# Optimization experiments

Hardware: AMD Instinct MI355X
Metric: run time of the kernel (lower is better)

Reference implementation:

```python
import jax, jax.numpy as jnp
import numpy as np
from functools import partial

B, E, H, M, NUM_NODES = 256, 256, 256, 128, 512


def _uni(key, shape, fan):
    bound = 1.0 / np.sqrt(fan)
    return jax.random.uniform(key, shape, jnp.float32, -bound, bound)


def setup_inputs() -> dict:
    key = jax.random.key(0)
    ks = jax.random.split(key, 12)
    return {
        "emb": jax.random.normal(ks[0], (B, E), jnp.float32),
        # FNN: Linear(E->H) + relu + Linear(H->H)  (num_layers=2, no batch norm)
        "fnn_w1": _uni(ks[1], (H, E), E),
        "fnn_b1": _uni(ks[2], (H,), E),
        "fnn_w2": _uni(ks[3], (H, H), H),
        "fnn_b2": _uni(ks[4], (H,), H),
        # GRUCell(input_size=H, hidden_size=H), torch layout: [3H, H] in (r,z,n) order
        "gru_w_ih": _uni(ks[5], (3 * H, H), H),
        "gru_b_ih": _uni(ks[6], (3 * H,), H),
        "gru_w_hh": _uni(ks[7], (3 * H, H), H),
        "gru_b_hh": _uni(ks[8], (3 * H,), H),
        # out_linear: Linear(H -> M)
        "out_w": _uni(ks[9], (M, H), H),
        "out_b": _uni(ks[10], (M,), H),
    }


def _gru_cell(x, h, w_ih, b_ih, w_hh, b_hh):
    # torch.nn.GRUCell math, gates in (r, z, n) order
    gi = x @ w_ih.T + b_ih            # [B, 3H]
    gh = h @ w_hh.T + b_hh            # [B, 3H]
    i_r, i_z, i_n = jnp.split(gi, 3, axis=-1)
    h_r, h_z, h_n = jnp.split(gh, 3, axis=-1)
    r = jax.nn.sigmoid(i_r + h_r)
    z = jax.nn.sigmoid(i_z + h_z)
    n = jnp.tanh(i_n + r * h_n)
    return (1.0 - z) * n + z * h


def reference(emb, fnn_w1, fnn_b1, fnn_w2, fnn_b2,
              gru_w_ih, gru_b_ih, gru_w_hh, gru_b_hh, out_w, out_b):
    # FNN: relu between layers, linear output
    hx = jax.nn.relu(emb @ fnn_w1.T + fnn_b1)
    hx = hx @ fnn_w2.T + fnn_b2                      # [B, H]

    cell = partial(_gru_cell, w_ih=gru_w_ih, b_ih=gru_b_ih,
                   w_hh=gru_w_hh, b_hh=gru_b_hh)

    def step(carry, _):
        h, prev_out = carry                           # input to cell is previous output
        h_new = cell(prev_out, h)
        return (h_new, h_new), h_new

    init = (hx, jnp.zeros_like(hx))                   # first input is zeros_like(hx)
    (hx_final, _), ys = jax.lax.scan(step, init, None, length=NUM_NODES)
    x = jnp.transpose(ys, (1, 0, 2))                  # [B, NUM_NODES, H]
    x = x @ out_w.T + out_b                           # [B, NUM_NODES, M]
    return (x, hx_final)
```

## Files before the change

### kernel.cpp

```cpp
#include <hip/hip_runtime.h>
#include <stdint.h>

#define BATCH 256
#define HDIM  256
#define MDIM  128
#define NSTEPS 512

typedef unsigned short u16;
typedef unsigned int   u32;
typedef unsigned long long u64;
typedef short short8 __attribute__((ext_vector_type(8)));
typedef float f32x4  __attribute__((ext_vector_type(4)));

__device__ __forceinline__ u16 f2bf(float f) {
    u32 x = __builtin_bit_cast(u32, f);
    u32 r = x + 0x7FFFu + ((x >> 16) & 1u);
    return (u16)(r >> 16);
}
__device__ __forceinline__ float bf2f(u16 h) {
    u32 x = ((u32)h) << 16;
    return __builtin_bit_cast(float, x);
}
__device__ __forceinline__ float sigm(float x) { return 1.f / (1.f + __expf(-x)); }
__device__ __forceinline__ float tanh_f(float x) {
    float ax = fabsf(x);
    float e  = __expf(-2.f * ax);
    float t  = (1.f - e) / (1.f + e);
    return copysignf(t, x);
}
__device__ __forceinline__ f32x4 mfma16(short8 a, short8 b, f32x4 c) {
    return __builtin_amdgcn_mfma_f32_16x16x32_bf16(a, b, c, 0, 0, 0);
}

__global__ __launch_bounds__(256) void k_prep(
    const float* __restrict__ w_ih, const float* __restrict__ w_hh,
    const float* __restrict__ b_ih, const float* __restrict__ b_hh,
    const float* __restrict__ ow,   const float* __restrict__ obv,
    u16* __restrict__ Whi, u16* __restrict__ Wlo, float* __restrict__ bias,
    u32* __restrict__ exch) {
    int row = blockIdx.x;
    int c   = threadIdx.x;
    float v;
    if (row < 512)        v = w_ih[row * HDIM + c] + w_hh[row * HDIM + c];
    else if (row < 768)   v = w_ih[row * HDIM + c];
    else if (row < 1024)  v = w_hh[(row - 256) * HDIM + c];
    else                  v = ow[(row - 1024) * HDIM + c];
    u16 hi = f2bf(v);
    u16 lo = f2bf(v - bf2f(hi));
    Whi[(size_t)row * HDIM + c] = hi;
    Wlo[(size_t)row * HDIM + c] = lo;
    if (c == 0) {
        float bv;
        if (row < 512)        bv = b_ih[row] + b_hh[row];
        else if (row < 768)   bv = b_ih[row];
        else if (row < 1024)  bv = b_hh[row - 256];
        else                  bv = obv[row - 1024];
        bias[row] = bv;
    }
    if (row < 512) exch[row * 256 + c] = 0u;
}

template <int RELU>
__global__ __launch_bounds__(256) void k_gemm_f32(
    const float* __restrict__ A, const float* __restrict__ W,
    const float* __restrict__ bvec, float* __restrict__ out, int N, int K) {
    __shared__ float At[16][17];
    __shared__ float Wt[16][17];
    int tx = threadIdx.x, ty = threadIdx.y;
    int mrow = blockIdx.x * 16 + ty;
    int nrow = blockIdx.y * 16 + ty;
    float acc = 0.0f;
    for (int k0 = 0; k0 < K; k0 += 16) {
        At[ty][tx] = A[(size_t)mrow * K + k0 + tx];
        Wt[ty][tx] = W[(size_t)nrow * K + k0 + tx];
        __syncthreads();
#pragma unroll
        for (int kk = 0; kk < 16; ++kk) acc += At[ty][kk] * Wt[tx][kk];
        __syncthreads();
    }
    int n = blockIdx.y * 16 + tx;
    float r = acc + bvec[n];
    if (RELU) r = fmaxf(r, 0.0f);
    out[(size_t)mrow * N + n] = r;
}

__global__ __launch_bounds__(64, 1) void k_scan(
    const u16* __restrict__ Whi, const u16* __restrict__ Wlo,
    const float* __restrict__ bias,
    const float* __restrict__ hx, const float* __restrict__ w_hh,
    const float* __restrict__ b_ih, const float* __restrict__ b_hh,
    u32* __restrict__ exch, float* __restrict__ out1, float* __restrict__ out2) {

    const int b    = blockIdx.x;
    const int w    = b >> 4;
    const int g    = b & 15;
    const int lane = threadIdx.x;
    const int col_l = lane & 15;
    const int kgrp  = lane >> 4;
    const int kofs  = kgrp * 8;
    const int r0    = kgrp * 4;
    const int jcol  = w * 16 + col_l;
    const int pcol  = (w & 7) * 16 + col_l;
    const int myt   = w >> 3;

    short8 bhi[4][8], blo[4][8], phi[8];
#pragma unroll
    for (int g4 = 0; g4 < 4; ++g4) {
        const u16* base_hi = Whi + (size_t)(g4 * 256 + jcol) * HDIM;
        const u16* base_lo = Wlo + (size_t)(g4 * 256 + jcol) * HDIM;
#pragma unroll
        for (int kt = 0; kt < 8; ++kt) {
            bhi[g4][kt] = *(const short8*)(base_hi + kt * 32 + kofs);
            blo[g4][kt] = *(const short8*)(base_lo + kt * 32 + kofs);
        }
    }
    {
        const u16* base_p = Whi + (size_t)(1024 + pcol) * HDIM;
#pragma unroll
        for (int kt = 0; kt < 8; ++kt)
            phi[kt] = *(const short8*)(base_p + kt * 32 + kofs);
    }

    const float b_r  = bias[jcol];
    const float b_z  = bias[256 + jcol];
    const float b_in = bias[512 + jcol];
    const float b_hn = bias[768 + jcol];
    const float ob   = bias[1024 + pcol];

    u32* const slab0 = exch + (size_t)(0 * 16 + g) * 4096;
    u32* const slab1 = exch + (size_t)(1 * 16 + g) * 4096;

    float hold[4];
    {
        float ghr[4] = {0, 0, 0, 0}, ghz[4] = {0, 0, 0, 0}, ghn[4] = {0, 0, 0, 0};
        const float* wr  = w_hh + (size_t)jcol * HDIM;
        const float* wz  = w_hh + (size_t)(256 + jcol) * HDIM;
        const float* wn  = w_hh + (size_t)(512 + jcol) * HDIM;
        const float* hx0 = hx + (size_t)(g * 16 + r0) * HDIM;
        for (int k = 0; k < HDIM; ++k) {
            float fr = wr[k], fz = wz[k], fn = wn[k];
#pragma unroll
            for (int i = 0; i < 4; ++i) {
                float h = hx0[i * HDIM + k];
                ghr[i] += h * fr; ghz[i] += h * fz; ghn[i] += h * fn;
            }
        }
        u32 p[4];
#pragma unroll
        for (int i = 0; i < 4; ++i) {
            float rr = sigm(b_ih[jcol] + b_hh[jcol] + ghr[i]);
            float zz = sigm(b_ih[256 + jcol] + b_hh[256 + jcol] + ghz[i]);
            float nn = tanh_f(b_ih[512 + jcol] + rr * (ghn[i] + b_hh[512 + jcol]));
            float hv = nn + zz * (hx0[i * HDIM + jcol] - nn);
            hold[i] = hv;
            p[i] = (1u << 16) | (u32)f2bf(hv);
        }
        u64* dst = (u64*)(slab1 + jcol * 16 + r0);
        __hip_atomic_store(&dst[0], ((u64)p[1] << 32) | p[0],
                           __ATOMIC_RELAXED, __HIP_MEMORY_SCOPE_AGENT);
        __hip_atomic_store(&dst[1], ((u64)p[3] << 32) | p[2],
                           __ATOMIC_RELAXED, __HIP_MEMORY_SCOPE_AGENT);
    }

    for (int s = 1; s <= 511; ++s) {
        const u32* ein = (s & 1) ? slab1 : slab0;
        u32*      eout = (s & 1) ? slab0 : slab1;
        const u32 tag  = (u32)s;

        short8 a[8];
        for (;;) {
            bool allok = true;
#pragma unroll
            for (int kt = 0; kt < 8; ++kt) {
                u32 v[8];
#pragma unroll
                for (int j = 0; j < 8; ++j)
                    v[j] = __hip_atomic_load(
                        ein + (kt * 32 + kofs + j) * 16 + col_l,
                        __ATOMIC_RELAXED, __HIP_MEMORY_SCOPE_AGENT);
#pragma unroll
                for (int j = 0; j < 8; ++j) {
                    allok = allok && ((v[j] >> 16) == tag);
                    a[kt][j] = (short)(v[j] & 0xFFFFu);
                }
            }
            if (__all((int)allok)) break;
            __builtin_amdgcn_s_sleep(1);
        }

        f32x4 acc[4];
#pragma unroll
        for (int n = 0; n < 4; ++n) acc[n] = (f32x4){0.f, 0.f, 0.f, 0.f};
#pragma unroll
        for (int kt = 0; kt < 8; ++kt) {
#pragma unroll
            for (int g4 = 0; g4 < 4; ++g4) {
                acc[g4] = mfma16(a[kt], bhi[g4][kt], acc[g4]);
                acc[g4] = mfma16(a[kt], blo[g4][kt], acc[g4]);
            }
        }

        u32 pk[4];
#pragma unroll
        for (int i = 0; i < 4; ++i) {
            float rr = sigm(acc[0][i] + b_r);
            float zz = sigm(acc[1][i] + b_z);
            float nn = tanh_f(acc[2][i] + b_in + rr * (acc[3][i] + b_hn));
            float hv = nn + zz * (hold[i] - nn);
            hold[i] = hv;
            pk[i] = ((u32)(s + 1) << 16) | (u32)f2bf(hv);
        }
        {
            u64* dst = (u64*)(eout + jcol * 16 + r0);
            __hip_atomic_store(&dst[0], ((u64)pk[1] << 32) | pk[0],
                               __ATOMIC_RELAXED, __HIP_MEMORY_SCOPE_AGENT);
            __hip_atomic_store(&dst[1], ((u64)pk[3] << 32) | pk[2],
                               __ATOMIC_RELAXED, __HIP_MEMORY_SCOPE_AGENT);
        }

        const int t = s - 1;
        if ((t & 1) == myt) {
            f32x4 oacc = (f32x4){0.f, 0.f, 0.f, 0.f};
#pragma unroll
            for (int kt = 0; kt < 8; ++kt) oacc = mfma16(a[kt], phi[kt], oacc);
#pragma unroll
            for (int i = 0; i < 4; ++i)
                out1[(size_t)(g * 16 + r0 + i) * (NSTEPS * MDIM) +
                     (size_t)t * MDIM + pcol] = oacc[i] + ob;
        }
    }

    if (myt == 1) {
        short8 a[8];
        for (;;) {
            bool allok = true;
#pragma unroll
            for (int kt = 0; kt < 8; ++kt) {
                u32 v[8];
#pragma unroll
                for (int j = 0; j < 8; ++j)
                    v[j] = __hip_atomic_load(
                        slab0 + (kt * 32 + kofs + j) * 16 + col_l,
                        __ATOMIC_RELAXED, __HIP_MEMORY_SCOPE_AGENT);
#pragma unroll
                for (int j = 0; j < 8; ++j) {
                    allok = allok && ((v[j] >> 16) == 512u);
                    a[kt][j] = (short)(v[j] & 0xFFFFu);
                }
            }
            if (__all((int)allok)) break;
            __builtin_amdgcn_s_sleep(1);
        }
        f32x4 oacc = (f32x4){0.f, 0.f, 0.f, 0.f};
#pragma unroll
        for (int kt = 0; kt < 8; ++kt) oacc = mfma16(a[kt], phi[kt], oacc);
#pragma unroll
        for (int i = 0; i < 4; ++i)
            out1[(size_t)(g * 16 + r0 + i) * (NSTEPS * MDIM) +
                 511ull * MDIM + pcol] = oacc[i] + ob;
    }

#pragma unroll
    for (int i = 0; i < 4; ++i)
        out2[(size_t)(g * 16 + r0 + i) * HDIM + jcol] = hold[i];
}

extern "C" void kernel_launch(void* const* d_in, const int* in_sizes, int n_in,
                              void* d_out, int out_size, void* d_ws, size_t ws_size,
                              hipStream_t stream) {
    const float* P[11];
    for (int i = 0; i < 11 && i < n_in; ++i) P[i] = (const float*)d_in[i];

    const float *emb, *w1, *b1, *w2, *b2, *w_ih, *b_ih, *w_hh, *b_hh, *ow, *obv;
    if (n_in > 1 && in_sizes[1] == 256) {
        emb = P[0]; b1 = P[1]; b2 = P[2]; w1 = P[3]; w2 = P[4];
        b_hh = P[5]; b_ih = P[6]; w_hh = P[7]; w_ih = P[8];
        obv = P[9]; ow = P[10];
    } else if (n_in > 1 && in_sizes[1] == 32768) {
        obv = P[0]; ow = P[1]; b_hh = P[2]; w_hh = P[3]; b_ih = P[4];
        w_ih = P[5]; b2 = P[6]; w2 = P[7]; b1 = P[8]; w1 = P[9]; emb = P[10];
    } else {
        emb = P[0]; w1 = P[1]; b1 = P[2]; w2 = P[3]; b2 = P[4];
        w_ih = P[5]; b_ih = P[6]; w_hh = P[7]; b_hh = P[8];
        ow = P[9]; obv = P[10];
    }

    float* out1 = (float*)d_out;
    float* out2 = out1 + (size_t)BATCH * NSTEPS * MDIM;

    char* ws = (char*)d_ws;
    u16*   Whi  = (u16*)(ws + 0);
    u16*   Wlo  = (u16*)(ws + 589824);
    float* bias = (float*)(ws + 1179648);
    u32*   exch = (u32*)(ws + 1184256);
    float* mid  = (float*)(ws + 1708544);
    float* hxb  = (float*)(ws + 1970688);

    k_prep<<<1152, 256, 0, stream>>>(w_ih, w_hh, b_ih, b_hh, ow, obv,
                                     Whi, Wlo, bias, exch);
    k_gemm_f32<1><<<dim3(16, 16), dim3(16, 16), 0, stream>>>(emb, w1, b1, mid, 256, 256);
    k_gemm_f32<0><<<dim3(16, 16), dim3(16, 16), 0, stream>>>(mid, w2, b2, hxb, 256, 256);
    k_scan<<<256, 64, 0, stream>>>(Whi, Wlo, bias, hxb, w_hh, b_ih, b_hh,
                                   exch, out1, out2);
}
```

Before: 1.755 ms.

## Interleave two batch groups per block and vectorize exchange spin loads

Each scan block now handles two independent batch groups (A and B) in alternation, halving the grid to 128 blocks. The idea is that while one group waits on the cross-block exchange, the other group's step overlaps with that latency. The exchange buffer layout is transposed so each lane reads contiguous dwordx4 words through inline-asm cache-bypassing loads with a single waitcnt, replacing many scalar atomic loads. The trade-off is that each block does twice the serial work per step, and having fewer blocks may lengthen the per-step critical path.

```diff
diff --git a/kernel.cpp b/kernel.cpp
--- a/kernel.cpp
+++ b/kernel.cpp
@@ -11,6 +11,7 @@
 typedef unsigned long long u64;
 typedef short short8 __attribute__((ext_vector_type(8)));
 typedef float f32x4  __attribute__((ext_vector_type(4)));
+typedef u32 u32x4 __attribute__((ext_vector_type(4)));
 
 __device__ __forceinline__ u16 f2bf(float f) {
     u32 x = __builtin_bit_cast(u32, f);
@@ -30,6 +31,40 @@
 }
 __device__ __forceinline__ f32x4 mfma16(short8 a, short8 b, f32x4 c) {
     return __builtin_amdgcn_mfma_f32_16x16x32_bf16(a, b, c, 0, 0, 0);
+}
+
+#define CLOAD16(dst, p, OFS)                                                   \
+    asm volatile("global_load_dwordx4 %0, %1, off offset:" OFS " sc0 sc1"      \
+                 : "=v"(dst) : "v"(p) : "memory")
+
+__device__ __forceinline__ void spin_load(const u32* base, u32 tag, short8 a[8]) {
+    for (;;) {
+        u32x4 v[16];
+        CLOAD16(v[0],  base, "0");   CLOAD16(v[1],  base, "16");
+        CLOAD16(v[2],  base, "128"); CLOAD16(v[3],  base, "144");
+        CLOAD16(v[4],  base, "256"); CLOAD16(v[5],  base, "272");
+        CLOAD16(v[6],  base, "384"); CLOAD16(v[7],  base, "400");
+        CLOAD16(v[8],  base, "512"); CLOAD16(v[9],  base, "528");
+        CLOAD16(v[10], base, "640"); CLOAD16(v[11], base, "656");
+        CLOAD16(v[12], base, "768"); CLOAD16(v[13], base, "784");
+        CLOAD16(v[14], base, "896"); CLOAD16(v[15], base, "912");
+        asm volatile("s_waitcnt vmcnt(0)" ::: "memory");
+        __builtin_amdgcn_sched_barrier(0);
+        bool ok = true;
+#pragma unroll
+        for (int i = 0; i < 16; ++i)
+#pragma unroll
+            for (int j = 0; j < 4; ++j) ok = ok && ((v[i][j] >> 16) == tag);
+        if (__all((int)ok)) {
+#pragma unroll
+            for (int kt = 0; kt < 8; ++kt)
+#pragma unroll
+                for (int j = 0; j < 8; ++j)
+                    a[kt][j] = (short)(v[2 * kt + (j >> 2)][j & 3] & 0xFFFFu);
+            return;
+        }
+        __builtin_amdgcn_s_sleep(1);
+    }
 }
 
 __global__ __launch_bounds__(256) void k_prep(
@@ -92,8 +127,10 @@
     u32* __restrict__ exch, float* __restrict__ out1, float* __restrict__ out2) {
 
     const int b    = blockIdx.x;
-    const int w    = b >> 4;
-    const int g    = b & 15;
+    const int w    = b >> 3;
+    const int p    = b & 7;
+    const int gA   = p;
+    const int gB   = p + 8;
     const int lane = threadIdx.x;
     const int col_l = lane & 15;
     const int kgrp  = lane >> 4;
@@ -127,142 +164,162 @@
     const float b_hn = bias[768 + jcol];
     const float ob   = bias[1024 + pcol];
 
-    u32* const slab0 = exch + (size_t)(0 * 16 + g) * 4096;
-    u32* const slab1 = exch + (size_t)(1 * 16 + g) * 4096;
-
-    float hold[4];
+    u32* const sA0 = exch + (size_t)(0 * 16 + gA) * 4096;
+    u32* const sA1 = exch + (size_t)(1 * 16 + gA) * 4096;
+    u32* const sB0 = exch + (size_t)(0 * 16 + gB) * 4096;
+    u32* const sB1 = exch + (size_t)(1 * 16 + gB) * 4096;
+    const int rd_off = col_l * 256 + kofs;
+    const int wr_off = r0 * 256 + jcol;
+
+    float holdA[4], holdB[4];
     {
-        float ghr[4] = {0, 0, 0, 0}, ghz[4] = {0, 0, 0, 0}, ghn[4] = {0, 0, 0, 0};
-        const float* wr  = w_hh + (size_t)jcol * HDIM;
-        const float* wz  = w_hh + (size_t)(256 + jcol) * HDIM;
-        const float* wn  = w_hh + (size_t)(512 + jcol) * HDIM;
-        const float* hx0 = hx + (size_t)(g * 16 + r0) * HDIM;
+        float gr[2][4] = {}, gz[2][4] = {}, gn[2][4] = {};
+        const float* wr_ = w_hh + (size_t)jcol * HDIM;
+        const float* wz_ = w_hh + (size_t)(256 + jcol) * HDIM;
+        const float* wn_ = w_hh + (size_t)(512 + jcol) * HDIM;
+        const float* hxA = hx + (size_t)(gA * 16 + r0) * HDIM;
+        const float* hxB = hx + (size_t)(gB * 16 + r0) * HDIM;
         for (int k = 0; k < HDIM; ++k) {
-            float fr = wr[k], fz = wz[k], fn = wn[k];
+            float fr = wr_[k], fz = wz_[k], fn = wn_[k];
 #pragma unroll
             for (int i = 0; i < 4; ++i) {
-                float h = hx0[i * HDIM + k];
-                ghr[i] += h * fr; ghz[i] += h * fz; ghn[i] += h * fn;
-            }
-        }
-        u32 p[4];
+                float hA = hxA[i * HDIM + k], hB = hxB[i * HDIM + k];
+                gr[0][i] += hA * fr; gz[0][i] += hA * fz; gn[0][i] += hA * fn;
+                gr[1][i] += hB * fr; gz[1][i] += hB * fz; gn[1][i] += hB * fn;
+            }
+        }
+        const float bi_r = b_ih[jcol] + b_hh[jcol];
+        const float bi_z = b_ih[256 + jcol] + b_hh[256 + jcol];
+        const float bi_n = b_ih[512 + jcol];
+        const float bh_n = b_hh[512 + jcol];
 #pragma unroll
         for (int i = 0; i < 4; ++i) {
-            float rr = sigm(b_ih[jcol] + b_hh[jcol] + ghr[i]);
-            float zz = sigm(b_ih[256 + jcol] + b_hh[256 + jcol] + ghz[i]);
-            float nn = tanh_f(b_ih[512 + jcol] + rr * (ghn[i] + b_hh[512 + jcol]));
-            float hv = nn + zz * (hx0[i * HDIM + jcol] - nn);
-            hold[i] = hv;
-            p[i] = (1u << 16) | (u32)f2bf(hv);
-        }
-        u64* dst = (u64*)(slab1 + jcol * 16 + r0);
-        __hip_atomic_store(&dst[0], ((u64)p[1] << 32) | p[0],
-                           __ATOMIC_RELAXED, __HIP_MEMORY_SCOPE_AGENT);
-        __hip_atomic_store(&dst[1], ((u64)p[3] << 32) | p[2],
-                           __ATOMIC_RELAXED, __HIP_MEMORY_SCOPE_AGENT);
+            float rr = sigm(bi_r + gr[0][i]);
+            float zz = sigm(bi_z + gz[0][i]);
+            float nn = tanh_f(bi_n + rr * (gn[0][i] + bh_n));
+            float hv = nn + zz * (hxA[i * HDIM + jcol] - nn);
+            holdA[i] = hv;
+            __hip_atomic_store(sA1 + wr_off + i * 256,
+                               (1u << 16) | (u32)f2bf(hv),
+                               __ATOMIC_RELAXED, __HIP_MEMORY_SCOPE_AGENT);
+        }
+#pragma unroll
+        for (int i = 0; i < 4; ++i) {
+            float rr = sigm(bi_r + gr[1][i]);
+            float zz = sigm(bi_z + gz[1][i]);
+            float nn = tanh_f(bi_n + rr * (gn[1][i] + bh_n));
+            float hv = nn + zz * (hxB[i * HDIM + jcol] - nn);
+            holdB[i] = hv;
+            __hip_atomic_store(sB1 + wr_off + i * 256,
+                               (1u << 16) | (u32)f2bf(hv),
+                               __ATOMIC_RELAXED, __HIP_MEMORY_SCOPE_AGENT);
+        }
     }
 
     for (int s = 1; s <= 511; ++s) {
-        const u32* ein = (s & 1) ? slab1 : slab0;
-        u32*      eout = (s & 1) ? slab0 : slab1;
-        const u32 tag  = (u32)s;
-
-        short8 a[8];
-        for (;;) {
-            bool allok = true;
-#pragma unroll
-            for (int kt = 0; kt < 8; ++kt) {
-                u32 v[8];
-#pragma unroll
-                for (int j = 0; j < 8; ++j)
-                    v[j] = __hip_atomic_load(
-                        ein + (kt * 32 + kofs + j) * 16 + col_l,
-                        __ATOMIC_RELAXED, __HIP_MEMORY_SCOPE_AGENT);
-#pragma unroll
-                for (int j = 0; j < 8; ++j) {
-                    allok = allok && ((v[j] >> 16) == tag);
-                    a[kt][j] = (short)(v[j] & 0xFFFFu);
+        const int pin  = s & 1;
+        const u32 tagN = (u32)(s + 1);
+        const int t    = s - 1;
+        const bool dop = ((t & 1) == myt);
+
+        {
+            const u32* ein = (pin ? sA1 : sA0) + rd_off;
+            u32*      eout = (pin ? sA0 : sA1) + wr_off;
+            short8 a[8];
+            spin_load(ein, (u32)s, a);
+            f32x4 acc[4];
+#pragma unroll
+            for (int n = 0; n < 4; ++n) acc[n] = (f32x4){0.f, 0.f, 0.f, 0.f};
+#pragma unroll
+            for (int kt = 0; kt < 8; ++kt)
+#pragma unroll
+                for (int g4 = 0; g4 < 4; ++g4) {
+                    acc[g4] = mfma16(a[kt], bhi[g4][kt], acc[g4]);
+                    acc[g4] = mfma16(a[kt], blo[g4][kt], acc[g4]);
                 }
-            }
-            if (__all((int)allok)) break;
-            __builtin_amdgcn_s_sleep(1);
-        }
-
-        f32x4 acc[4];
-#pragma unroll
-        for (int n = 0; n < 4; ++n) acc[n] = (f32x4){0.f, 0.f, 0.f, 0.f};
-#pragma unroll
-        for (int kt = 0; kt < 8; ++kt) {
-#pragma unroll
-            for (int g4 = 0; g4 < 4; ++g4) {
-                acc[g4] = mfma16(a[kt], bhi[g4][kt], acc[g4]);
-                acc[g4] = mfma16(a[kt], blo[g4][kt], acc[g4]);
-            }
-        }
-
-        u32 pk[4];
-#pragma unroll
-        for (int i = 0; i < 4; ++i) {
-            float rr = sigm(acc[0][i] + b_r);
-            float zz = sigm(acc[1][i] + b_z);
-            float nn = tanh_f(acc[2][i] + b_in + rr * (acc[3][i] + b_hn));
-            float hv = nn + zz * (hold[i] - nn);
-            hold[i] = hv;
-            pk[i] = ((u32)(s + 1) << 16) | (u32)f2bf(hv);
-        }
+#pragma unroll
+            for (int i = 0; i < 4; ++i) {
+                float rr = sigm(acc[0][i] + b_r);
+                float zz = sigm(acc[1][i] + b_z);
+                float nn = tanh_f(acc[2][i] + b_in + rr * (acc[3][i] + b_hn));
+                float hv = nn + zz * (holdA[i] - nn);
+                holdA[i] = hv;
+                __hip_atomic_store(eout + i * 256, (tagN << 16) | (u32)f2bf(hv),
+                                   __ATOMIC_RELAXED, __HIP_MEMORY_SCOPE_AGENT);
+            }
+            if (dop) {
+                f32x4 oacc = (f32x4){0.f, 0.f, 0.f, 0.f};
+#pragma unroll
+                for (int kt = 0; kt < 8; ++kt) oacc = mfma16(a[kt], phi[kt], oacc);
+#pragma unroll
+                for (int i = 0; i < 4; ++i)
+                    out1[(size_t)(gA * 16 + r0 + i) * (NSTEPS * MDIM) +
+                         (size_t)t * MDIM + pcol] = oacc[i] + ob;
+            }
+        }
+
         {
-            u64* dst = (u64*)(eout + jcol * 16 + r0);
-            __hip_atomic_store(&dst[0], ((u64)pk[1] << 32) | pk[0],
-                               __ATOMIC_RELAXED, __HIP_MEMORY_SCOPE_AGENT);
-            __hip_atomic_store(&dst[1], ((u64)pk[3] << 32) | pk[2],
-                               __ATOMIC_RELAXED, __HIP_MEMORY_SCOPE_AGENT);
-        }
-
-        const int t = s - 1;
-        if ((t & 1) == myt) {
-            f32x4 oacc = (f32x4){0.f, 0.f, 0.f, 0.f};
-#pragma unroll
-            for (int kt = 0; kt < 8; ++kt) oacc = mfma16(a[kt], phi[kt], oacc);
-#pragma unroll
-            for (int i = 0; i < 4; ++i)
-                out1[(size_t)(g * 16 + r0 + i) * (NSTEPS * MDIM) +
-                     (size_t)t * MDIM + pcol] = oacc[i] + ob;
+            const u32* ein = (pin ? sB1 : sB0) + rd_off;
+            u32*      eout = (pin ? sB0 : sB1) + wr_off;
+            short8 a[8];
+            spin_load(ein, (u32)s, a);
+            f32x4 acc[4];
+#pragma unroll
+            for (int n = 0; n < 4; ++n) acc[n] = (f32x4){0.f, 0.f, 0.f, 0.f};
+#pragma unroll
+            for (int kt = 0; kt < 8; ++kt)
+#pragma unroll
+                for (int g4 = 0; g4 < 4; ++g4) {
+                    acc[g4] = mfma16(a[kt], bhi[g4][kt], acc[g4]);
+                    acc[g4] = mfma16(a[kt], blo[g4][kt], acc[g4]);
+                }
+#pragma unroll
+            for (int i = 0; i < 4; ++i) {
+                float rr = sigm(acc[0][i] + b_r);
+                float zz = sigm(acc[1][i] + b_z);
+                float nn = tanh_f(acc[2][i] + b_in + rr * (acc[3][i] + b_hn));
+                float hv = nn + zz * (holdB[i] - nn);
+                holdB[i] = hv;
+                __hip_atomic_store(eout + i * 256, (tagN << 16) | (u32)f2bf(hv),
+                                   __ATOMIC_RELAXED, __HIP_MEMORY_SCOPE_AGENT);
+            }
+            if (dop) {
+                f32x4 oacc = (f32x4){0.f, 0.f, 0.f, 0.f};
+#pragma unroll
+                for (int kt = 0; kt < 8; ++kt) oacc = mfma16(a[kt], phi[kt], oacc);
+#pragma unroll
+                for (int i = 0; i < 4; ++i)
+                    out1[(size_t)(gB * 16 + r0 + i) * (NSTEPS * MDIM) +
+                         (size_t)t * MDIM + pcol] = oacc[i] + ob;
+            }
         }
     }
 
     if (myt == 1) {
         short8 a[8];
-        for (;;) {
-            bool allok = true;
-#pragma unroll
-            for (int kt = 0; kt < 8; ++kt) {
-                u32 v[8];
-#pragma unroll
-                for (int j = 0; j < 8; ++j)
-                    v[j] = __hip_atomic_load(
-                        slab0 + (kt * 32 + kofs + j) * 16 + col_l,
-                        __ATOMIC_RELAXED, __HIP_MEMORY_SCOPE_AGENT);
-#pragma unroll
-                for (int j = 0; j < 8; ++j) {
-                    allok = allok && ((v[j] >> 16) == 512u);
-                    a[kt][j] = (short)(v[j] & 0xFFFFu);
-                }
-            }
-            if (__all((int)allok)) break;
-            __builtin_amdgcn_s_sleep(1);
-        }
+        spin_load(sA0 + rd_off, 512u, a);
         f32x4 oacc = (f32x4){0.f, 0.f, 0.f, 0.f};
 #pragma unroll
         for (int kt = 0; kt < 8; ++kt) oacc = mfma16(a[kt], phi[kt], oacc);
 #pragma unroll
         for (int i = 0; i < 4; ++i)
-            out1[(size_t)(g * 16 + r0 + i) * (NSTEPS * MDIM) +
+            out1[(size_t)(gA * 16 + r0 + i) * (NSTEPS * MDIM) +
                  511ull * MDIM + pcol] = oacc[i] + ob;
-    }
-
-#pragma unroll
-    for (int i = 0; i < 4; ++i)
-        out2[(size_t)(g * 16 + r0 + i) * HDIM + jcol] = hold[i];
+        spin_load(sB0 + rd_off, 512u, a);
+        oacc = (f32x4){0.f, 0.f, 0.f, 0.f};
+#pragma unroll
+        for (int kt = 0; kt < 8; ++kt) oacc = mfma16(a[kt], phi[kt], oacc);
+#pragma unroll
+        for (int i = 0; i < 4; ++i)
+            out1[(size_t)(gB * 16 + r0 + i) * (NSTEPS * MDIM) +
+                 511ull * MDIM + pcol] = oacc[i] + ob;
+    }
+
+#pragma unroll
+    for (int i = 0; i < 4; ++i) {
+        out2[(size_t)(gA * 16 + r0 + i) * HDIM + jcol] = holdA[i];
+        out2[(size_t)(gB * 16 + r0 + i) * HDIM + jcol] = holdB[i];
+    }
 }
 
 extern "C" void kernel_launch(void* const* d_in, const int* in_sizes, int n_in,
@@ -300,6 +357,6 @@
                                      Whi, Wlo, bias, exch);
     k_gemm_f32<1><<<dim3(16, 16), dim3(16, 16), 0, stream>>>(emb, w1, b1, mid, 256, 256);
     k_gemm_f32<0><<<dim3(16, 16), dim3(16, 16), 0, stream>>>(mid, w2, b2, hxb, 256, 256);
-    k_scan<<<256, 64, 0, stream>>>(Whi, Wlo, bias, hxb, w_hh, b_ih, b_hh,
+    k_scan<<<128, 64, 0, stream>>>(Whi, Wlo, bias, hxb, w_hh, b_ih, b_hh,
                                    exch, out1, out2);
 }
```

After: 2.716 ms. 54.7% more time.

## Restructure GRU scan exchange with vectorized cache-bypassing loads and deferred output stores

Applied to the files above, without the earlier changes.

Changes the exchange slab layout so each lane reads its 64 K-values as sixteen contiguous dwordx4 loads, replacing 64 scalar atomic loads, and writes with scalar sc0 sc1 stores. The spin loop polls at L2 scope and only occasionally at system scope with a sleep. Output-projection stores are deferred to the next step so they leave the critical path, and the workgroup-to-batch-group mapping is permuted, presumably to spread groups across XCDs. The visibility semantics now rely on cache-control bits in inline asm, which risks stale reads or coherence problems across XCDs.

```diff
diff --git a/kernel.cpp b/kernel.cpp
--- a/kernel.cpp
+++ b/kernel.cpp
@@ -8,9 +8,9 @@
 
 typedef unsigned short u16;
 typedef unsigned int   u32;
-typedef unsigned long long u64;
 typedef short short8 __attribute__((ext_vector_type(8)));
 typedef float f32x4  __attribute__((ext_vector_type(4)));
+typedef u32 u32x4 __attribute__((ext_vector_type(4)));
 
 __device__ __forceinline__ u16 f2bf(float f) {
     u32 x = __builtin_bit_cast(u32, f);
@@ -30,6 +30,51 @@
 }
 __device__ __forceinline__ f32x4 mfma16(short8 a, short8 b, f32x4 c) {
     return __builtin_amdgcn_mfma_f32_16x16x32_bf16(a, b, c, 0, 0, 0);
+}
+
+#define CLOAD_L2(dst, p, OFS)                                                  \
+    asm volatile("global_load_dwordx4 %0, %1, off offset:" OFS " sc0"          \
+                 : "=v"(dst) : "v"(p) : "memory")
+#define CLOAD_SYS(dst, p, OFS)                                                 \
+    asm volatile("global_load_dwordx4 %0, %1, off offset:" OFS " sc0 sc1"      \
+                 : "=v"(dst) : "v"(p) : "memory")
+#define CSTORE(p, v)                                                           \
+    asm volatile("global_store_dword %0, %1, off sc0 sc1"                      \
+                 :: "v"(p), "v"(v) : "memory")
+
+#define ISSUE16(MACRO, v, base)                                                \
+    MACRO(v[0],  base, "0");   MACRO(v[1],  base, "16");                       \
+    MACRO(v[2],  base, "128"); MACRO(v[3],  base, "144");                      \
+    MACRO(v[4],  base, "256"); MACRO(v[5],  base, "272");                      \
+    MACRO(v[6],  base, "384"); MACRO(v[7],  base, "400");                      \
+    MACRO(v[8],  base, "512"); MACRO(v[9],  base, "528");                      \
+    MACRO(v[10], base, "640"); MACRO(v[11], base, "656");                      \
+    MACRO(v[12], base, "768"); MACRO(v[13], base, "784");                      \
+    MACRO(v[14], base, "896"); MACRO(v[15], base, "912")
+
+__device__ __forceinline__ void spin_load(const u32* base, u32 tag, short8 a[8]) {
+    for (int it = 0;; ++it) {
+        u32x4 v[16];
+        const bool sys = ((it & 3) == 3);
+        if (sys) { ISSUE16(CLOAD_SYS, v, base); }
+        else     { ISSUE16(CLOAD_L2,  v, base); }
+        asm volatile("s_waitcnt vmcnt(0)" ::: "memory");
+        __builtin_amdgcn_sched_barrier(0);
+        bool ok = true;
+#pragma unroll
+        for (int i = 0; i < 16; ++i)
+#pragma unroll
+            for (int j = 0; j < 4; ++j) ok = ok && ((v[i][j] >> 16) == tag);
+        if (__all((int)ok)) {
+#pragma unroll
+            for (int kt = 0; kt < 8; ++kt)
+#pragma unroll
+                for (int j = 0; j < 8; ++j)
+                    a[kt][j] = (short)(v[2 * kt + (j >> 2)][j & 3] & 0xFFFFu);
+            return;
+        }
+        if (sys) __builtin_amdgcn_s_sleep(1);
+    }
 }
 
 __global__ __launch_bounds__(256) void k_prep(
@@ -93,7 +138,7 @@
 
     const int b    = blockIdx.x;
     const int w    = b >> 4;
-    const int g    = b & 15;
+    const int g    = ((b & 7) << 1) | ((b >> 3) & 1);
     const int lane = threadIdx.x;
     const int col_l = lane & 15;
     const int kgrp  = lane >> 4;
@@ -129,23 +174,24 @@
 
     u32* const slab0 = exch + (size_t)(0 * 16 + g) * 4096;
     u32* const slab1 = exch + (size_t)(1 * 16 + g) * 4096;
+    const int rd_off = col_l * 256 + kofs;
+    const int wr_off = r0 * 256 + jcol;
 
     float hold[4];
     {
         float ghr[4] = {0, 0, 0, 0}, ghz[4] = {0, 0, 0, 0}, ghn[4] = {0, 0, 0, 0};
-        const float* wr  = w_hh + (size_t)jcol * HDIM;
-        const float* wz  = w_hh + (size_t)(256 + jcol) * HDIM;
-        const float* wn  = w_hh + (size_t)(512 + jcol) * HDIM;
+        const float* wr_ = w_hh + (size_t)jcol * HDIM;
+        const float* wz_ = w_hh + (size_t)(256 + jcol) * HDIM;
+        const float* wn_ = w_hh + (size_t)(512 + jcol) * HDIM;
         const float* hx0 = hx + (size_t)(g * 16 + r0) * HDIM;
         for (int k = 0; k < HDIM; ++k) {
-            float fr = wr[k], fz = wz[k], fn = wn[k];
+            float fr = wr_[k], fz = wz_[k], fn = wn_[k];
 #pragma unroll
             for (int i = 0; i < 4; ++i) {
                 float h = hx0[i * HDIM + k];
                 ghr[i] += h * fr; ghz[i] += h * fz; ghn[i] += h * fn;
             }
         }
-        u32 p[4];
 #pragma unroll
         for (int i = 0; i < 4; ++i) {
             float rr = sigm(b_ih[jcol] + b_hh[jcol] + ghr[i]);
@@ -153,54 +199,39 @@
             float nn = tanh_f(b_ih[512 + jcol] + rr * (ghn[i] + b_hh[512 + jcol]));
             float hv = nn + zz * (hx0[i * HDIM + jcol] - nn);
             hold[i] = hv;
-            p[i] = (1u << 16) | (u32)f2bf(hv);
-        }
-        u64* dst = (u64*)(slab1 + jcol * 16 + r0);
-        __hip_atomic_store(&dst[0], ((u64)p[1] << 32) | p[0],
-                           __ATOMIC_RELAXED, __HIP_MEMORY_SCOPE_AGENT);
-        __hip_atomic_store(&dst[1], ((u64)p[3] << 32) | p[2],
-                           __ATOMIC_RELAXED, __HIP_MEMORY_SCOPE_AGENT);
-    }
-
+            CSTORE(slab1 + wr_off + i * 256, (1u << 16) | (u32)f2bf(hv));
+        }
+    }
+
+    f32x4 opend;
+    int   tpend = -1;
     for (int s = 1; s <= 511; ++s) {
-        const u32* ein = (s & 1) ? slab1 : slab0;
-        u32*      eout = (s & 1) ? slab0 : slab1;
-        const u32 tag  = (u32)s;
+        const u32* ein = ((s & 1) ? slab1 : slab0) + rd_off;
+        u32*      eout = ((s & 1) ? slab0 : slab1) + wr_off;
 
         short8 a[8];
-        for (;;) {
-            bool allok = true;
-#pragma unroll
-            for (int kt = 0; kt < 8; ++kt) {
-                u32 v[8];
-#pragma unroll
-                for (int j = 0; j < 8; ++j)
-                    v[j] = __hip_atomic_load(
-                        ein + (kt * 32 + kofs + j) * 16 + col_l,
-                        __ATOMIC_RELAXED, __HIP_MEMORY_SCOPE_AGENT);
-#pragma unroll
-                for (int j = 0; j < 8; ++j) {
-                    allok = allok && ((v[j] >> 16) == tag);
-                    a[kt][j] = (short)(v[j] & 0xFFFFu);
-                }
-            }
-            if (__all((int)allok)) break;
-            __builtin_amdgcn_s_sleep(1);
+        spin_load(ein, (u32)s, a);
+
+        if (tpend >= 0) {
+#pragma unroll
+            for (int i = 0; i < 4; ++i)
+                __builtin_nontemporal_store(
+                    opend[i] + ob,
+                    out1 + (size_t)(g * 16 + r0 + i) * (NSTEPS * MDIM) +
+                        (size_t)tpend * MDIM + pcol);
         }
 
         f32x4 acc[4];
 #pragma unroll
         for (int n = 0; n < 4; ++n) acc[n] = (f32x4){0.f, 0.f, 0.f, 0.f};
 #pragma unroll
-        for (int kt = 0; kt < 8; ++kt) {
+        for (int kt = 0; kt < 8; ++kt)
 #pragma unroll
             for (int g4 = 0; g4 < 4; ++g4) {
                 acc[g4] = mfma16(a[kt], bhi[g4][kt], acc[g4]);
                 acc[g4] = mfma16(a[kt], blo[g4][kt], acc[g4]);
             }
-        }
-
-        u32 pk[4];
+
 #pragma unroll
         for (int i = 0; i < 4; ++i) {
             float rr = sigm(acc[0][i] + b_r);
@@ -208,14 +239,7 @@
             float nn = tanh_f(acc[2][i] + b_in + rr * (acc[3][i] + b_hn));
             float hv = nn + zz * (hold[i] - nn);
             hold[i] = hv;
-            pk[i] = ((u32)(s + 1) << 16) | (u32)f2bf(hv);
-        }
-        {
-            u64* dst = (u64*)(eout + jcol * 16 + r0);
-            __hip_atomic_store(&dst[0], ((u64)pk[1] << 32) | pk[0],
-                               __ATOMIC_RELAXED, __HIP_MEMORY_SCOPE_AGENT);
-            __hip_atomic_store(&dst[1], ((u64)pk[3] << 32) | pk[2],
-                               __ATOMIC_RELAXED, __HIP_MEMORY_SCOPE_AGENT);
+            CSTORE(eout + i * 256, ((u32)(s + 1) << 16) | (u32)f2bf(hv));
         }
 
         const int t = s - 1;
@@ -223,46 +247,38 @@
             f32x4 oacc = (f32x4){0.f, 0.f, 0.f, 0.f};
 #pragma unroll
             for (int kt = 0; kt < 8; ++kt) oacc = mfma16(a[kt], phi[kt], oacc);
-#pragma unroll
-            for (int i = 0; i < 4; ++i)
-                out1[(size_t)(g * 16 + r0 + i) * (NSTEPS * MDIM) +
-                     (size_t)t * MDIM + pcol] = oacc[i] + ob;
-        }
+            opend = oacc;
+            tpend = t;
+        }
+    }
+
+    if (tpend >= 0) {
+#pragma unroll
+        for (int i = 0; i < 4; ++i)
+            __builtin_nontemporal_store(
+                opend[i] + ob,
+                out1 + (size_t)(g * 16 + r0 + i) * (NSTEPS * MDIM) +
+                    (size_t)tpend * MDIM + pcol);
     }
 
     if (myt == 1) {
         short8 a[8];
-        for (;;) {
-            bool allok = true;
-#pragma unroll
-            for (int kt = 0; kt < 8; ++kt) {
-                u32 v[8];
-#pragma unroll
-                for (int j = 0; j < 8; ++j)
-                    v[j] = __hip_atomic_load(
-                        slab0 + (kt * 32 + kofs + j) * 16 + col_l,
-                        __ATOMIC_RELAXED, __HIP_MEMORY_SCOPE_AGENT);
-#pragma unroll
-                for (int j = 0; j < 8; ++j) {
-                    allok = allok && ((v[j] >> 16) == 512u);
-                    a[kt][j] = (short)(v[j] & 0xFFFFu);
-                }
-            }
-            if (__all((int)allok)) break;
-            __builtin_amdgcn_s_sleep(1);
-        }
+        spin_load(slab0 + rd_off, 512u, a);
         f32x4 oacc = (f32x4){0.f, 0.f, 0.f, 0.f};
 #pragma unroll
         for (int kt = 0; kt < 8; ++kt) oacc = mfma16(a[kt], phi[kt], oacc);
 #pragma unroll
         for (int i = 0; i < 4; ++i)
-            out1[(size_t)(g * 16 + r0 + i) * (NSTEPS * MDIM) +
-                 511ull * MDIM + pcol] = oacc[i] + ob;
+            __builtin_nontemporal_store(
+                oacc[i] + ob,
+                out1 + (size_t)(g * 16 + r0 + i) * (NSTEPS * MDIM) +
+                    511ull * MDIM + pcol);
     }
 
 #pragma unroll
     for (int i = 0; i < 4; ++i)
-        out2[(size_t)(g * 16 + r0 + i) * HDIM + jcol] = hold[i];
+        __builtin_nontemporal_store(
+            hold[i], out2 + (size_t)(g * 16 + r0 + i) * HDIM + jcol);
 }
 
 extern "C" void kernel_launch(void* const* d_in, const int* in_sizes, int n_in,
```

Result: slower. 2.990 ms (+70.4%).
